# Performance work log

Measured on AMD Instinct MI355X. Metric: run time of the kernel, lower is better.

## Reference

```python
import jax, jax.numpy as jnp
import numpy as np

NUM_GRAPHS = 5 * 0 + 64  # number of graphs in the batch
NUM_CLASSES = 5


def gcn_conv(x, src, dst, W, b, n_nodes):
    """PyG GCNConv: x' = D^{-1/2} (A+I) D^{-1/2} x W + b (self-loops already in src/dst)."""
    h = x @ W  # [N, out]
    deg = jax.ops.segment_sum(jnp.ones(dst.shape, h.dtype), dst, num_segments=n_nodes)
    dinv = deg ** -0.5  # deg >= 1 thanks to self-loops
    norm = dinv[src] * dinv[dst]  # [E+N]
    msg = h[src] * norm[:, None]  # gather + normalize
    out = jax.ops.segment_sum(msg, dst, num_segments=n_nodes)  # scatter-add
    return out + b


def setup_inputs() -> dict:
    key = jax.random.key(0)
    ks = jax.random.split(key, 12)
    N, E, D_IN, D_H, D_F = 50000, 500000, 128, 256, 256
    x = jax.random.normal(ks[0], (N, D_IN), dtype=jnp.float32)
    edge_index = jax.random.randint(ks[1], (2, E), 0, N, dtype=jnp.int64)
    batch = jnp.sort(jax.random.randint(ks[2], (N,), 0, NUM_GRAPHS, dtype=jnp.int64))
    def lin(k, fi, fo):
        s = 1.0 / np.sqrt(fi)
        return jax.random.uniform(k, (fi, fo), jnp.float32, -s, s)
    return {
        "x": x, "edge_index": edge_index, "batch": batch,
        "W0": lin(ks[3], D_IN, D_H), "b0": jnp.zeros((D_H,), jnp.float32),
        "W1": lin(ks[4], D_H, D_H),  "b1": jnp.zeros((D_H,), jnp.float32),
        "W2": lin(ks[5], D_H, D_H),  "b2": jnp.zeros((D_H,), jnp.float32),
        "Wc1": lin(ks[6], D_H, D_F), "bc1": jnp.zeros((D_F,), jnp.float32),
        "Wc2": lin(ks[7], D_F, NUM_CLASSES), "bc2": jnp.zeros((NUM_CLASSES,), jnp.float32),
    }


def reference(x, edge_index, batch, W0, b0, W1, b1, W2, b2, Wc1, bc1, Wc2, bc2):
    n_nodes = x.shape[0]
    loops = jnp.arange(n_nodes, dtype=edge_index.dtype)
    src = jnp.concatenate([edge_index[0], loops])
    dst = jnp.concatenate([edge_index[1], loops])

    h = jax.nn.relu(gcn_conv(x, src, dst, W0, b0, n_nodes))
    h = jax.nn.relu(gcn_conv(h, src, dst, W1, b1, n_nodes))
    h = jax.nn.relu(gcn_conv(h, src, dst, W2, b2, n_nodes))

    # global_mean_pool over batch ids
    sums = jax.ops.segment_sum(h, batch, num_segments=NUM_GRAPHS)
    cnts = jax.ops.segment_sum(jnp.ones((n_nodes,), h.dtype), batch, num_segments=NUM_GRAPHS)
    g = sums / jnp.maximum(cnts, 1.0)[:, None]  # [NUM_GRAPHS, D_H]

    # classifier MLP (dropout inactive at eval)
    out = jax.nn.relu(g @ Wc1 + bc1) @ Wc2 + bc2
    return out
```

## Files before the change

### kernel.cpp

```cpp
#include <hip/hip_runtime.h>
#include <hip/hip_fp16.h>

typedef short s16x8 __attribute__((ext_vector_type(8)));
typedef float fx4 __attribute__((ext_vector_type(4)));

#define AS_G(p) ((const __attribute__((address_space(1))) void*)(p))
#define AS_L(p) ((__attribute__((address_space(3))) void*)(p))

struct __align__(8) half4 { __half2 lo, hi; };

__device__ inline unsigned short f32_to_bf16(float f) {
    unsigned int u = __float_as_uint(f);
    return (unsigned short)((u + 0x7fffu + ((u >> 16) & 1u)) >> 16);
}
__device__ inline float bf16_to_f32(unsigned short b) {
    return __uint_as_float(((unsigned int)b) << 16);
}
__device__ inline void split2(float a, unsigned short& hi, unsigned short& lo) {
    hi = f32_to_bf16(a);
    lo = f32_to_bf16(a - bf16_to_f32(hi));
}


__global__ void k_degx(const int* __restrict__ dst, int E, int* __restrict__ deg, int degB,
                       const float* __restrict__ x, __half* __restrict__ xh, int nx) {
    if (blockIdx.x < (unsigned)degB) {
        int i = blockIdx.x * 256 + threadIdx.x;
        if (i < E) atomicAdd(&deg[dst[i]], 1);
    } else {
        int i = (blockIdx.x - degB) * 1024 + threadIdx.x * 4;
        if (i < nx) {
            float4 v = *(const float4*)&x[i];
            __half2 h0(__float2half(v.x), __float2half(v.y));
            __half2 h1(__float2half(v.z), __float2half(v.w));
            *(__half2*)&xh[i] = h0;
            *(__half2*)&xh[i + 2] = h1;
        }
    }
}

__global__ void k_scan1w(const int* __restrict__ deg, int N, int nb,
                         int* __restrict__ part, int* __restrict__ bsum, float* __restrict__ dinv,
                         const float* __restrict__ W0, unsigned short* __restrict__ h0, unsigned short* __restrict__ l0,
                         const float* __restrict__ W1, unsigned short* __restrict__ h1, unsigned short* __restrict__ l1,
                         const float* __restrict__ W2, unsigned short* __restrict__ h2, unsigned short* __restrict__ l2,
                         int DIN, int DH) {
    __shared__ int s[256];
    if (blockIdx.x < (unsigned)nb) {
        int i = blockIdx.x * 256 + threadIdx.x;
        int v = (i < N) ? deg[i] : 0;
        if (i < N) dinv[i] = 1.0f / sqrtf((float)(v + 1));
        s[threadIdx.x] = v;
        __syncthreads();
        for (int off = 1; off < 256; off <<= 1) {
            int t = (threadIdx.x >= off) ? s[threadIdx.x - off] : 0;
            __syncthreads();
            s[threadIdx.x] += t;
            __syncthreads();
        }
        if (i < N) part[i] = s[threadIdx.x] - v;
        if (threadIdx.x == 255) bsum[blockIdx.x] = s[255];
    } else {
        int i = (blockIdx.x - nb) * 256 + threadIdx.x;
        const int n0 = DIN * DH, n1 = DH * DH;
        const float* W; unsigned short *hT, *lT; int K, li;
        if (i < n0) { W = W0; hT = h0; lT = l0; K = DIN; li = i; }
        else if (i < n0 + n1) { W = W1; hT = h1; lT = l1; K = DH; li = i - n0; }
        else if (i < n0 + 2 * n1) { W = W2; hT = h2; lT = l2; K = DH; li = i - n0 - n1; }
        else return;
        int k = li / DH, n = li - k * DH;
        unsigned short h, l;
        split2(W[li], h, l);
        hT[(size_t)n * K + k] = h;
        lT[(size_t)n * K + k] = l;
    }
}

__global__ void k_scan3(const int* __restrict__ part, const int* __restrict__ bsum, int nb,
                        int N, int E, int* __restrict__ rowptr, int* __restrict__ cursor) {
    __shared__ int s[256];
    const int t = threadIdx.x;
    s[t] = (t < nb && t < (int)blockIdx.x) ? bsum[t] : 0;
    __syncthreads();
    for (int off = 128; off > 0; off >>= 1) {
        if (t < off) s[t] += s[t + off];
        __syncthreads();
    }
    const int base = s[0];
    int i = blockIdx.x * 256 + t;
    if (i < N) {
        int v = part[i] + base;
        rowptr[i] = v;
        cursor[i] = v;
    }
    if (i == 0) rowptr[N] = E;
}

__global__ void k_fill(const int* __restrict__ src, const int* __restrict__ dst, int E,
                       const float* __restrict__ dinv, int* __restrict__ cursor,
                       int* __restrict__ col, float* __restrict__ nrm) {
    int e = blockIdx.x * blockDim.x + threadIdx.x;
    if (e < E) {
        int s = src[e], d = dst[e];
        int p = atomicAdd(&cursor[d], 1);
        col[p] = s;
        nrm[p] = dinv[s] * dinv[d];
    }
}


__global__ __launch_bounds__(256) void k_gemm_mfma(
    const unsigned short* __restrict__ Ahi, const unsigned short* __restrict__ Alo,
    const unsigned short* __restrict__ BhiT, const unsigned short* __restrict__ BloT,
    const float* __restrict__ bias, __half* __restrict__ C, int Nrows, int K) {
    __shared__ __align__(16) unsigned short smem[2][4][128 * 32];

    const int tid = threadIdx.x;
    const int wid = tid >> 6, lane = tid & 63;
    const int row0 = blockIdx.y * 128;
    const int col0 = blockIdx.x * 128;
    const int wrow = wid & 1, wcol = wid >> 1;
    const int quad = lane >> 4, l16 = lane & 15;

    const unsigned short* garr = (wid == 0) ? Ahi : (wid == 1) ? Alo : (wid == 2) ? BhiT : BloT;
    const bool isA = (wid < 2);

    const unsigned short* gp[8];
#pragma unroll
    for (int i = 0; i < 8; ++i) {
        int r = 16 * i + (lane >> 2);
        int s = lane & 3;
        int q = (s - (r >> 1)) & 3;
        int grow = isA ? min(row0 + r, Nrows - 1) : (col0 + r);
        gp[i] = garr + (size_t)grow * K + q * 8;
    }

    int aidx[4], bidx[4];
#pragma unroll
    for (int t = 0; t < 4; ++t) {
        int ra = wrow * 64 + t * 16 + l16;
        aidx[t] = ra * 32 + ((quad + (ra >> 1)) & 3) * 8;
        int rb = wcol * 64 + t * 16 + l16;
        bidx[t] = rb * 32 + ((quad + (rb >> 1)) & 3) * 8;
    }

    fx4 acc[4][4] = {};
    const int nch = K / 32;

#pragma unroll
    for (int i = 0; i < 8; ++i)
        __builtin_amdgcn_global_load_lds(AS_G(gp[i]), AS_L((char*)smem[0][wid] + i * 1024), 16, 0, 0);
    __syncthreads();

    for (int t = 0; t < nch; ++t) {
        const int buf = t & 1;
        if (t + 1 < nch) {
#pragma unroll
            for (int i = 0; i < 8; ++i)
                __builtin_amdgcn_global_load_lds(AS_G(gp[i] + (t + 1) * 32),
                                                 AS_L((char*)smem[1 - buf][wid] + i * 1024), 16, 0, 0);
        }

        const unsigned short* sAhi = smem[buf][0];
        const unsigned short* sAlo = smem[buf][1];
        const unsigned short* sBhi = smem[buf][2];
        const unsigned short* sBlo = smem[buf][3];

        s16x8 ah[4], al[4];
#pragma unroll
        for (int mi = 0; mi < 4; ++mi) {
            ah[mi] = *(const s16x8*)&sAhi[aidx[mi]];
            al[mi] = *(const s16x8*)&sAlo[aidx[mi]];
        }
#pragma unroll
        for (int nj = 0; nj < 4; ++nj) {
            s16x8 bh = *(const s16x8*)&sBhi[bidx[nj]];
            s16x8 bl = *(const s16x8*)&sBlo[bidx[nj]];
#pragma unroll
            for (int mi = 0; mi < 4; ++mi) {
                acc[mi][nj] = __builtin_amdgcn_mfma_f32_16x16x32_bf16(ah[mi], bh, acc[mi][nj], 0, 0, 0);
                acc[mi][nj] = __builtin_amdgcn_mfma_f32_16x16x32_bf16(ah[mi], bl, acc[mi][nj], 0, 0, 0);
                acc[mi][nj] = __builtin_amdgcn_mfma_f32_16x16x32_bf16(al[mi], bh, acc[mi][nj], 0, 0, 0);
            }
        }
        if (t + 1 < nch) __syncthreads();
    }

#pragma unroll
    for (int mi = 0; mi < 4; ++mi) {
        const int rbase = row0 + wrow * 64 + mi * 16 + quad * 4;
#pragma unroll
        for (int nj = 0; nj < 4; ++nj) {
            const int c = col0 + wcol * 64 + nj * 16 + l16;
            const float bc = bias[c];
#pragma unroll
            for (int reg = 0; reg < 4; ++reg) {
                int r = rbase + reg;
                if (r < Nrows) C[(size_t)r * 256 + c] = __float2half(fmaxf(acc[mi][nj][reg] + bc, 0.f));
            }
        }
    }
}

__global__ __launch_bounds__(256) void k_gemm_pool(
    const unsigned short* __restrict__ Ahi, const unsigned short* __restrict__ Alo,
    const unsigned short* __restrict__ BhiT, const unsigned short* __restrict__ BloT,
    const float* __restrict__ bias, const int* __restrict__ batch,
    float* __restrict__ gsum, int Nrows, int K) {
    __shared__ __align__(16) unsigned short smem[2][4][128 * 32];

    const int tid = threadIdx.x;
    const int wid = tid >> 6, lane = tid & 63;
    const int row0 = blockIdx.y * 128;
    const int col0 = blockIdx.x * 128;
    const int wrow = wid & 1, wcol = wid >> 1;
    const int quad = lane >> 4, l16 = lane & 15;

    const unsigned short* garr = (wid == 0) ? Ahi : (wid == 1) ? Alo : (wid == 2) ? BhiT : BloT;
    const bool isA = (wid < 2);

    const unsigned short* gp[8];
#pragma unroll
    for (int i = 0; i < 8; ++i) {
        int r = 16 * i + (lane >> 2);
        int s = lane & 3;
        int q = (s - (r >> 1)) & 3;
        int grow = isA ? min(row0 + r, Nrows - 1) : (col0 + r);
        gp[i] = garr + (size_t)grow * K + q * 8;
    }

    int aidx[4], bidx[4];
#pragma unroll
    for (int t = 0; t < 4; ++t) {
        int ra = wrow * 64 + t * 16 + l16;
        aidx[t] = ra * 32 + ((quad + (ra >> 1)) & 3) * 8;
        int rb = wcol * 64 + t * 16 + l16;
        bidx[t] = rb * 32 + ((quad + (rb >> 1)) & 3) * 8;
    }

    fx4 acc[4][4] = {};
    const int nch = K / 32;

#pragma unroll
    for (int i = 0; i < 8; ++i)
        __builtin_amdgcn_global_load_lds(AS_G(gp[i]), AS_L((char*)smem[0][wid] + i * 1024), 16, 0, 0);
    __syncthreads();

    for (int t = 0; t < nch; ++t) {
        const int buf = t & 1;
        if (t + 1 < nch) {
#pragma unroll
            for (int i = 0; i < 8; ++i)
                __builtin_amdgcn_global_load_lds(AS_G(gp[i] + (t + 1) * 32),
                                                 AS_L((char*)smem[1 - buf][wid] + i * 1024), 16, 0, 0);
        }

        const unsigned short* sAhi = smem[buf][0];
        const unsigned short* sAlo = smem[buf][1];
        const unsigned short* sBhi = smem[buf][2];
        const unsigned short* sBlo = smem[buf][3];

        s16x8 ah[4], al[4];
#pragma unroll
        for (int mi = 0; mi < 4; ++mi) {
            ah[mi] = *(const s16x8*)&sAhi[aidx[mi]];
            al[mi] = *(const s16x8*)&sAlo[aidx[mi]];
        }
#pragma unroll
        for (int nj = 0; nj < 4; ++nj) {
            s16x8 bh = *(const s16x8*)&sBhi[bidx[nj]];
            s16x8 bl = *(const s16x8*)&sBlo[bidx[nj]];
#pragma unroll
            for (int mi = 0; mi < 4; ++mi) {
                acc[mi][nj] = __builtin_amdgcn_mfma_f32_16x16x32_bf16(ah[mi], bh, acc[mi][nj], 0, 0, 0);
                acc[mi][nj] = __builtin_amdgcn_mfma_f32_16x16x32_bf16(ah[mi], bl, acc[mi][nj], 0, 0, 0);
                acc[mi][nj] = __builtin_amdgcn_mfma_f32_16x16x32_bf16(al[mi], bh, acc[mi][nj], 0, 0, 0);
            }
        }
        if (t + 1 < nch) __syncthreads();
    }

    int bg[4][4];
#pragma unroll
    for (int mi = 0; mi < 4; ++mi)
#pragma unroll
        for (int reg = 0; reg < 4; ++reg) {
            int r = row0 + wrow * 64 + mi * 16 + quad * 4 + reg;
            bg[mi][reg] = (r < Nrows) ? batch[r] : -1;
        }
    const int gfirst = batch[row0 < Nrows ? row0 : (Nrows - 1)];
    const int glast  = batch[min(row0 + 127, Nrows - 1)];

#pragma unroll
    for (int nj = 0; nj < 4; ++nj) {
        const int c = col0 + wcol * 64 + nj * 16 + l16;
        const float bc = bias[c];
        for (int g = gfirst; g <= glast; ++g) {
            float s = 0.f;
#pragma unroll
            for (int mi = 0; mi < 4; ++mi)
#pragma unroll
                for (int reg = 0; reg < 4; ++reg)
                    if (bg[mi][reg] == g) s += fmaxf(acc[mi][nj][reg] + bc, 0.f);
            s += __shfl_xor(s, 16);
            s += __shfl_xor(s, 32);
            if (quad == 0) atomicAdd(&gsum[g * 256 + c], s);
        }
    }
}


__global__ __launch_bounds__(256) void k_agg256(const __half* __restrict__ H, const int* __restrict__ rowptr,
                                                const int* __restrict__ col, const float* __restrict__ nrm,
                                                const float* __restrict__ dinv,
                                                unsigned short* __restrict__ outHi,
                                                unsigned short* __restrict__ outLo, int N) {
    const int wave = threadIdx.x >> 6, lane = threadIdx.x & 63;
    const int v = blockIdx.x * 4 + wave;
    if (v >= N) return;

    const float di = dinv[v];
    const float selfn = di * di;
    half4 hv = ((const half4*)&H[(size_t)v * 256])[lane];
    float2 s0 = __half22float2(hv.lo), s1 = __half22float2(hv.hi);
    float ax = selfn * s0.x, ay = selfn * s0.y, az = selfn * s1.x, aw = selfn * s1.y;

    int e = rowptr[v];
    const int end = rowptr[v + 1];
    for (; e + 8 <= end; e += 8) {
        int u[8]; float w[8]; half4 g[8];
#pragma unroll
        for (int j = 0; j < 8; ++j) { u[j] = col[e + j]; w[j] = nrm[e + j]; }
#pragma unroll
        for (int j = 0; j < 8; ++j) g[j] = ((const half4*)&H[(size_t)u[j] * 256])[lane];
#pragma unroll
        for (int j = 0; j < 8; ++j) {
            float2 f0 = __half22float2(g[j].lo), f1 = __half22float2(g[j].hi);
            ax += w[j] * f0.x; ay += w[j] * f0.y; az += w[j] * f1.x; aw += w[j] * f1.y;
        }
    }
    for (; e < end; ++e) {
        const int u = col[e];
        const float w = nrm[e];
        half4 g = ((const half4*)&H[(size_t)u * 256])[lane];
        float2 f0 = __half22float2(g.lo), f1 = __half22float2(g.hi);
        ax += w * f0.x; ay += w * f0.y; az += w * f1.x; aw += w * f1.y;
    }

    ushort4 hi4, lo4;
    split2(ax, hi4.x, lo4.x);
    split2(ay, hi4.y, lo4.y);
    split2(az, hi4.z, lo4.z);
    split2(aw, hi4.w, lo4.w);
    ((ushort4*)outHi)[(size_t)v * 64 + lane] = hi4;
    ((ushort4*)outLo)[(size_t)v * 64 + lane] = lo4;
}

__global__ __launch_bounds__(256) void k_agg128(const __half* __restrict__ X, const int* __restrict__ rowptr,
                                                const int* __restrict__ col, const float* __restrict__ nrm,
                                                const float* __restrict__ dinv,
                                                unsigned short* __restrict__ outHi,
                                                unsigned short* __restrict__ outLo, int N) {
    const int half = threadIdx.x >> 5, sub = threadIdx.x & 31;
    const int v = blockIdx.x * 8 + half;
    if (v >= N) return;

    const float di = dinv[v];
    const float selfn = di * di;
    half4 hv = ((const half4*)&X[(size_t)v * 128])[sub];
    float2 s0 = __half22float2(hv.lo), s1 = __half22float2(hv.hi);
    float ax = selfn * s0.x, ay = selfn * s0.y, az = selfn * s1.x, aw = selfn * s1.y;

    int e = rowptr[v];
    const int end = rowptr[v + 1];
    for (; e + 4 <= end; e += 4) {
        int u[4]; float w[4]; half4 g[4];
#pragma unroll
        for (int j = 0; j < 4; ++j) { u[j] = col[e + j]; w[j] = nrm[e + j]; }
#pragma unroll
        for (int j = 0; j < 4; ++j) g[j] = ((const half4*)&X[(size_t)u[j] * 128])[sub];
#pragma unroll
        for (int j = 0; j < 4; ++j) {
            float2 f0 = __half22float2(g[j].lo), f1 = __half22float2(g[j].hi);
            ax += w[j] * f0.x; ay += w[j] * f0.y; az += w[j] * f1.x; aw += w[j] * f1.y;
        }
    }
    for (; e < end; ++e) {
        const int u = col[e];
        const float w = nrm[e];
        half4 g = ((const half4*)&X[(size_t)u * 128])[sub];
        float2 f0 = __half22float2(g.lo), f1 = __half22float2(g.hi);
        ax += w * f0.x; ay += w * f0.y; az += w * f1.x; aw += w * f1.y;
    }

    ushort4 hi4, lo4;
    split2(ax, hi4.x, lo4.x);
    split2(ay, hi4.y, lo4.y);
    split2(az, hi4.z, lo4.z);
    split2(aw, hi4.w, lo4.w);
    ((ushort4*)outHi)[(size_t)v * 32 + sub] = hi4;
    ((ushort4*)outLo)[(size_t)v * 32 + sub] = lo4;
}


__global__ __launch_bounds__(256) void k_poolcls(const float* __restrict__ gsum, const int* __restrict__ batch,
                                                 int N,
                                                 const float* __restrict__ Wc1, const float* __restrict__ bc1,
                                                 const float* __restrict__ Wc2, const float* __restrict__ bc2,
                                                 float* __restrict__ out) {
    __shared__ float sg[256], sh[256];
    __shared__ int bounds[2];
    const int b = blockIdx.x, t = threadIdx.x;
    if (t < 2) {
        int target = b + t;
        int lo = 0, hi = N;
        while (lo < hi) {
            int mid = (lo + hi) >> 1;
            if (batch[mid] < target) lo = mid + 1; else hi = mid;
        }
        bounds[t] = lo;
    }
    __syncthreads();
    const float c = (float)(bounds[1] - bounds[0]);
    sg[t] = gsum[b * 256 + t] / fmaxf(c, 1.0f);
    __syncthreads();
    float acc = bc1[t];
    for (int k = 0; k < 256; ++k) acc += sg[k] * Wc1[k * 256 + t];
    sh[t] = fmaxf(acc, 0.f);
    __syncthreads();
    if (t < 5) {
        float o = bc2[t];
        for (int k = 0; k < 256; ++k) o += sh[k] * Wc2[k * 5 + t];
        out[b * 5 + t] = o;
    }
}


extern "C" void kernel_launch(void* const* d_in, const int* in_sizes, int n_in,
                              void* d_out, int out_size, void* d_ws, size_t ws_size,
                              hipStream_t stream) {
    const float* x    = (const float*)d_in[0];
    const int*   eidx = (const int*)d_in[1];
    const int*   batch= (const int*)d_in[2];
    const float* W0 = (const float*)d_in[3];  const float* b0 = (const float*)d_in[4];
    const float* W1 = (const float*)d_in[5];  const float* b1 = (const float*)d_in[6];
    const float* W2 = (const float*)d_in[7];  const float* b2 = (const float*)d_in[8];
    const float* Wc1= (const float*)d_in[9];  const float* bc1= (const float*)d_in[10];
    const float* Wc2= (const float*)d_in[11]; const float* bc2= (const float*)d_in[12];
    float* out = (float*)d_out;

    const int N   = in_sizes[2];
    const int E   = in_sizes[1] / 2;
    const int DIN = in_sizes[0] / N;
    const int DH  = in_sizes[4];
    const int* src = eidx;
    const int* dst = eidx + E;

    char* p = (char*)d_ws;
    auto alloc = [&](size_t bytes) {
        char* r = p;
        p += (bytes + 255) & ~(size_t)255;
        return (void*)r;
    };
    __half*         hbuf = (__half*)alloc((size_t)N * DH * 2);
    __half*         xh   = (__half*)alloc((size_t)N * DIN * 2);
    unsigned short* hhi  = (unsigned short*)alloc((size_t)N * DH * 2);
    unsigned short* hlo  = (unsigned short*)alloc((size_t)N * DH * 2);
    unsigned short* w0hi = (unsigned short*)alloc((size_t)DH * DIN * 2);
    unsigned short* w0lo = (unsigned short*)alloc((size_t)DH * DIN * 2);
    unsigned short* w1hi = (unsigned short*)alloc((size_t)DH * DH * 2);
    unsigned short* w1lo = (unsigned short*)alloc((size_t)DH * DH * 2);
    unsigned short* w2hi = (unsigned short*)alloc((size_t)DH * DH * 2);
    unsigned short* w2lo = (unsigned short*)alloc((size_t)DH * DH * 2);
    int*   deg   = (int*)alloc((size_t)N * 4);
    float* gsum  = (float*)alloc(64 * (size_t)DH * 4);
    float* dinv  = (float*)alloc((size_t)N * 4);
    int*   part  = (int*)alloc((size_t)N * 4);
    int*   bsum  = (int*)alloc(256 * 4);
    int*   rowptr= (int*)alloc((size_t)(N + 1) * 4);
    int*   cursor= (int*)alloc((size_t)N * 4);
    int*   col   = (int*)alloc((size_t)E * 4);
    float* nrm   = (float*)alloc((size_t)E * 4);

    hipMemsetAsync(deg, 0, (size_t)((char*)gsum - (char*)deg) + 64 * (size_t)DH * 4, stream);

    const int nb = (N + 255) / 256;
    const int wtot = DIN * DH + 2 * DH * DH;
    const int wb = (wtot + 255) / 256;
    const int degB = (E + 255) / 256;
    const int nx = N * DIN;
    const int xb = (nx + 1023) / 1024;

    k_degx  <<<degB + xb, 256, 0, stream>>>(dst, E, deg, degB, x, xh, nx);
    k_scan1w<<<nb + wb, 256, 0, stream>>>(deg, N, nb, part, bsum, dinv,
                                          W0, w0hi, w0lo, W1, w1hi, w1lo, W2, w2hi, w2lo, DIN, DH);
    k_scan3 <<<nb, 256, 0, stream>>>(part, bsum, nb, N, E, rowptr, cursor);
    k_fill  <<<(E + 255) / 256, 256, 0, stream>>>(src, dst, E, dinv, cursor, col, nrm);

    dim3 gemmGrid(DH / 128, (N + 127) / 128);

    k_agg128<<<(N + 7) / 8, 256, 0, stream>>>(xh, rowptr, col, nrm, dinv, hhi, hlo, N);
    k_gemm_mfma<<<gemmGrid, 256, 0, stream>>>(hhi, hlo, w0hi, w0lo, b0, hbuf, N, DIN);
    k_agg256<<<(N + 3) / 4, 256, 0, stream>>>(hbuf, rowptr, col, nrm, dinv, hhi, hlo, N);
    k_gemm_mfma<<<gemmGrid, 256, 0, stream>>>(hhi, hlo, w1hi, w1lo, b1, hbuf, N, DH);
    k_agg256<<<(N + 3) / 4, 256, 0, stream>>>(hbuf, rowptr, col, nrm, dinv, hhi, hlo, N);
    k_gemm_pool<<<gemmGrid, 256, 0, stream>>>(hhi, hlo, w2hi, w2lo, b2, batch, gsum, N, DH);

    k_poolcls<<<64, 256, 0, stream>>>(gsum, batch, N, Wc1, bc1, Wc2, bc2, out);
}
```

Measured before the change: 398.6 us.

## Switch GEMMs to fp16 with single-precision activations and split weights

Replaces the bf16 three-term split (Ahi*Bhi + Ahi*Blo + Alo*Bhi) with fp16 MFMA. Activations are kept as a single fp16 array and only the weights are split into hi/lo, so each step issues two MFMAs instead of three. The aggregation kernels now write one fp16 activation array instead of hi and lo arrays, which halves that write traffic and the GEMM's A-operand reads. The shared GEMM core drops the double-buffered LDS prefetch for a single buffer with load, sync, compute, sync, so global-load latency is no longer overlapped with compute, and accuracy now relies on fp16 activation precision.

```diff
diff --git a/kernel.cpp b/kernel.cpp
--- a/kernel.cpp
+++ b/kernel.cpp
@@ -1,7 +1,7 @@
 #include <hip/hip_runtime.h>
 #include <hip/hip_fp16.h>
 
-typedef short s16x8 __attribute__((ext_vector_type(8)));
+typedef _Float16 f16x8 __attribute__((ext_vector_type(8)));
 typedef float fx4 __attribute__((ext_vector_type(4)));
 
 #define AS_G(p) ((const __attribute__((address_space(1))) void*)(p))
@@ -9,16 +9,9 @@
 
 struct __align__(8) half4 { __half2 lo, hi; };
 
-__device__ inline unsigned short f32_to_bf16(float f) {
-    unsigned int u = __float_as_uint(f);
-    return (unsigned short)((u + 0x7fffu + ((u >> 16) & 1u)) >> 16);
-}
-__device__ inline float bf16_to_f32(unsigned short b) {
-    return __uint_as_float(((unsigned int)b) << 16);
-}
-__device__ inline void split2(float a, unsigned short& hi, unsigned short& lo) {
-    hi = f32_to_bf16(a);
-    lo = f32_to_bf16(a - bf16_to_f32(hi));
+__device__ inline void split2h(float a, __half& hi, __half& lo) {
+    hi = __float2half(a);
+    lo = __float2half(a - __half2float(hi));
 }
 
 
@@ -41,9 +34,9 @@
 
 __global__ void k_scan1w(const int* __restrict__ deg, int N, int nb,
                          int* __restrict__ part, int* __restrict__ bsum, float* __restrict__ dinv,
-                         const float* __restrict__ W0, unsigned short* __restrict__ h0, unsigned short* __restrict__ l0,
-                         const float* __restrict__ W1, unsigned short* __restrict__ h1, unsigned short* __restrict__ l1,
-                         const float* __restrict__ W2, unsigned short* __restrict__ h2, unsigned short* __restrict__ l2,
+                         const float* __restrict__ W0, __half* __restrict__ h0, __half* __restrict__ l0,
+                         const float* __restrict__ W1, __half* __restrict__ h1, __half* __restrict__ l1,
+                         const float* __restrict__ W2, __half* __restrict__ h2, __half* __restrict__ l2,
                          int DIN, int DH) {
     __shared__ int s[256];
     if (blockIdx.x < (unsigned)nb) {
@@ -63,14 +56,14 @@
     } else {
         int i = (blockIdx.x - nb) * 256 + threadIdx.x;
         const int n0 = DIN * DH, n1 = DH * DH;
-        const float* W; unsigned short *hT, *lT; int K, li;
+        const float* W; __half *hT, *lT; int K, li;
         if (i < n0) { W = W0; hT = h0; lT = l0; K = DIN; li = i; }
         else if (i < n0 + n1) { W = W1; hT = h1; lT = l1; K = DH; li = i - n0; }
         else if (i < n0 + 2 * n1) { W = W2; hT = h2; lT = l2; K = DH; li = i - n0 - n1; }
         else return;
         int k = li / DH, n = li - k * DH;
-        unsigned short h, l;
-        split2(W[li], h, l);
+        __half h, l;
+        split2h(W[li], h, l);
         hT[(size_t)n * K + k] = h;
         lT[(size_t)n * K + k] = l;
     }
@@ -109,31 +102,28 @@
 }
 
 
-__global__ __launch_bounds__(256) void k_gemm_mfma(
-    const unsigned short* __restrict__ Ahi, const unsigned short* __restrict__ Alo,
-    const unsigned short* __restrict__ BhiT, const unsigned short* __restrict__ BloT,
-    const float* __restrict__ bias, __half* __restrict__ C, int Nrows, int K) {
-    __shared__ __align__(16) unsigned short smem[2][4][128 * 32];
-
-    const int tid = threadIdx.x;
-    const int wid = tid >> 6, lane = tid & 63;
-    const int row0 = blockIdx.y * 128;
-    const int col0 = blockIdx.x * 128;
-    const int wrow = wid & 1, wcol = wid >> 1;
-    const int quad = lane >> 4, l16 = lane & 15;
-
-    const unsigned short* garr = (wid == 0) ? Ahi : (wid == 1) ? Alo : (wid == 2) ? BhiT : BloT;
-    const bool isA = (wid < 2);
-
-    const unsigned short* gp[8];
-#pragma unroll
-    for (int i = 0; i < 8; ++i) {
-        int r = 16 * i + (lane >> 2);
+__device__ __forceinline__ void gemm_core(
+    const __half* __restrict__ Aop, const __half* __restrict__ BhiT, const __half* __restrict__ BloT,
+    __half* smem, int Nrows, int K, int row0, int col0,
+    int wid, int lane, int wrow, int wcol, int quad, int l16, fx4 (&acc)[4][4]) {
+    const __half* gp[6];
+    int ldsoff[6];
+#pragma unroll
+    for (int j = 0; j < 6; ++j) {
+        int L = wid * 6 + j;
+        int arr = L >> 3, slot = L & 7;
+        int r = 16 * slot + (lane >> 2);
         int s = lane & 3;
         int q = (s - (r >> 1)) & 3;
-        int grow = isA ? min(row0 + r, Nrows - 1) : (col0 + r);
-        gp[i] = garr + (size_t)grow * K + q * 8;
-    }
+        const __half* garr = (arr == 0) ? Aop : (arr == 1) ? BhiT : BloT;
+        int grow = (arr == 0) ? min(row0 + r, Nrows - 1) : (col0 + r);
+        gp[j] = garr + (size_t)grow * K + q * 8;
+        ldsoff[j] = arr * 8192 + slot * 1024;
+    }
+
+    const __half* sA   = smem;
+    const __half* sBhi = smem + 128 * 32;
+    const __half* sBlo = smem + 2 * 128 * 32;
 
     int aidx[4], bidx[4];
 #pragma unroll
@@ -144,47 +134,41 @@
         bidx[t] = rb * 32 + ((quad + (rb >> 1)) & 3) * 8;
     }
 
+    for (int k0 = 0; k0 < K; k0 += 32) {
+#pragma unroll
+        for (int j = 0; j < 6; ++j)
+            __builtin_amdgcn_global_load_lds(AS_G(gp[j] + k0), AS_L((char*)smem + ldsoff[j]), 16, 0, 0);
+        __syncthreads();
+
+        f16x8 a[4];
+#pragma unroll
+        for (int mi = 0; mi < 4; ++mi) a[mi] = *(const f16x8*)&sA[aidx[mi]];
+#pragma unroll
+        for (int nj = 0; nj < 4; ++nj) {
+            f16x8 bh = *(const f16x8*)&sBhi[bidx[nj]];
+            f16x8 bl = *(const f16x8*)&sBlo[bidx[nj]];
+#pragma unroll
+            for (int mi = 0; mi < 4; ++mi) {
+                acc[mi][nj] = __builtin_amdgcn_mfma_f32_16x16x32_f16(a[mi], bh, acc[mi][nj], 0, 0, 0);
+                acc[mi][nj] = __builtin_amdgcn_mfma_f32_16x16x32_f16(a[mi], bl, acc[mi][nj], 0, 0, 0);
+            }
+        }
+        __syncthreads();
+    }
+}
+
+__global__ __launch_bounds__(256) void k_gemm_mfma(
+    const __half* __restrict__ Aop, const __half* __restrict__ BhiT, const __half* __restrict__ BloT,
+    const float* __restrict__ bias, __half* __restrict__ C, int Nrows, int K) {
+    __shared__ __align__(16) __half smem[3 * 128 * 32];
+    const int tid = threadIdx.x;
+    const int wid = tid >> 6, lane = tid & 63;
+    const int row0 = blockIdx.y * 128, col0 = blockIdx.x * 128;
+    const int wrow = wid & 1, wcol = wid >> 1;
+    const int quad = lane >> 4, l16 = lane & 15;
+
     fx4 acc[4][4] = {};
-    const int nch = K / 32;
-
-#pragma unroll
-    for (int i = 0; i < 8; ++i)
-        __builtin_amdgcn_global_load_lds(AS_G(gp[i]), AS_L((char*)smem[0][wid] + i * 1024), 16, 0, 0);
-    __syncthreads();
-
-    for (int t = 0; t < nch; ++t) {
-        const int buf = t & 1;
-        if (t + 1 < nch) {
-#pragma unroll
-            for (int i = 0; i < 8; ++i)
-                __builtin_amdgcn_global_load_lds(AS_G(gp[i] + (t + 1) * 32),
-                                                 AS_L((char*)smem[1 - buf][wid] + i * 1024), 16, 0, 0);
-        }
-
-        const unsigned short* sAhi = smem[buf][0];
-        const unsigned short* sAlo = smem[buf][1];
-        const unsigned short* sBhi = smem[buf][2];
-        const unsigned short* sBlo = smem[buf][3];
-
-        s16x8 ah[4], al[4];
-#pragma unroll
-        for (int mi = 0; mi < 4; ++mi) {
-            ah[mi] = *(const s16x8*)&sAhi[aidx[mi]];
-            al[mi] = *(const s16x8*)&sAlo[aidx[mi]];
-        }
-#pragma unroll
-        for (int nj = 0; nj < 4; ++nj) {
-            s16x8 bh = *(const s16x8*)&sBhi[bidx[nj]];
-            s16x8 bl = *(const s16x8*)&sBlo[bidx[nj]];
-#pragma unroll
-            for (int mi = 0; mi < 4; ++mi) {
-                acc[mi][nj] = __builtin_amdgcn_mfma_f32_16x16x32_bf16(ah[mi], bh, acc[mi][nj], 0, 0, 0);
-                acc[mi][nj] = __builtin_amdgcn_mfma_f32_16x16x32_bf16(ah[mi], bl, acc[mi][nj], 0, 0, 0);
-                acc[mi][nj] = __builtin_amdgcn_mfma_f32_16x16x32_bf16(al[mi], bh, acc[mi][nj], 0, 0, 0);
-            }
-        }
-        if (t + 1 < nch) __syncthreads();
-    }
+    gemm_core(Aop, BhiT, BloT, smem, Nrows, K, row0, col0, wid, lane, wrow, wcol, quad, l16, acc);
 
 #pragma unroll
     for (int mi = 0; mi < 4; ++mi) {
@@ -203,82 +187,18 @@
 }
 
 __global__ __launch_bounds__(256) void k_gemm_pool(
-    const unsigned short* __restrict__ Ahi, const unsigned short* __restrict__ Alo,
-    const unsigned short* __restrict__ BhiT, const unsigned short* __restrict__ BloT,
+    const __half* __restrict__ Aop, const __half* __restrict__ BhiT, const __half* __restrict__ BloT,
     const float* __restrict__ bias, const int* __restrict__ batch,
     float* __restrict__ gsum, int Nrows, int K) {
-    __shared__ __align__(16) unsigned short smem[2][4][128 * 32];
-
+    __shared__ __align__(16) __half smem[3 * 128 * 32];
     const int tid = threadIdx.x;
     const int wid = tid >> 6, lane = tid & 63;
-    const int row0 = blockIdx.y * 128;
-    const int col0 = blockIdx.x * 128;
+    const int row0 = blockIdx.y * 128, col0 = blockIdx.x * 128;
     const int wrow = wid & 1, wcol = wid >> 1;
     const int quad = lane >> 4, l16 = lane & 15;
 
-    const unsigned short* garr = (wid == 0) ? Ahi : (wid == 1) ? Alo : (wid == 2) ? BhiT : BloT;
-    const bool isA = (wid < 2);
-
-    const unsigned short* gp[8];
-#pragma unroll
-    for (int i = 0; i < 8; ++i) {
-        int r = 16 * i + (lane >> 2);
-        int s = lane & 3;
-        int q = (s - (r >> 1)) & 3;
-        int grow = isA ? min(row0 + r, Nrows - 1) : (col0 + r);
-        gp[i] = garr + (size_t)grow * K + q * 8;
-    }
-
-    int aidx[4], bidx[4];
-#pragma unroll
-    for (int t = 0; t < 4; ++t) {
-        int ra = wrow * 64 + t * 16 + l16;
-        aidx[t] = ra * 32 + ((quad + (ra >> 1)) & 3) * 8;
-        int rb = wcol * 64 + t * 16 + l16;
-        bidx[t] = rb * 32 + ((quad + (rb >> 1)) & 3) * 8;
-    }
-
     fx4 acc[4][4] = {};
-    const int nch = K / 32;
-
-#pragma unroll
-    for (int i = 0; i < 8; ++i)
-        __builtin_amdgcn_global_load_lds(AS_G(gp[i]), AS_L((char*)smem[0][wid] + i * 1024), 16, 0, 0);
-    __syncthreads();
-
-    for (int t = 0; t < nch; ++t) {
-        const int buf = t & 1;
-        if (t + 1 < nch) {
-#pragma unroll
-            for (int i = 0; i < 8; ++i)
-                __builtin_amdgcn_global_load_lds(AS_G(gp[i] + (t + 1) * 32),
-                                                 AS_L((char*)smem[1 - buf][wid] + i * 1024), 16, 0, 0);
-        }
-
-        const unsigned short* sAhi = smem[buf][0];
-        const unsigned short* sAlo = smem[buf][1];
-        const unsigned short* sBhi = smem[buf][2];
-        const unsigned short* sBlo = smem[buf][3];
-
-        s16x8 ah[4], al[4];
-#pragma unroll
-        for (int mi = 0; mi < 4; ++mi) {
-            ah[mi] = *(const s16x8*)&sAhi[aidx[mi]];
-            al[mi] = *(const s16x8*)&sAlo[aidx[mi]];
-        }
-#pragma unroll
-        for (int nj = 0; nj < 4; ++nj) {
-            s16x8 bh = *(const s16x8*)&sBhi[bidx[nj]];
-            s16x8 bl = *(const s16x8*)&sBlo[bidx[nj]];
-#pragma unroll
-            for (int mi = 0; mi < 4; ++mi) {
-                acc[mi][nj] = __builtin_amdgcn_mfma_f32_16x16x32_bf16(ah[mi], bh, acc[mi][nj], 0, 0, 0);
-                acc[mi][nj] = __builtin_amdgcn_mfma_f32_16x16x32_bf16(ah[mi], bl, acc[mi][nj], 0, 0, 0);
-                acc[mi][nj] = __builtin_amdgcn_mfma_f32_16x16x32_bf16(al[mi], bh, acc[mi][nj], 0, 0, 0);
-            }
-        }
-        if (t + 1 < nch) __syncthreads();
-    }
+    gemm_core(Aop, BhiT, BloT, smem, Nrows, K, row0, col0, wid, lane, wrow, wcol, quad, l16, acc);
 
     int bg[4][4];
 #pragma unroll
@@ -313,8 +233,7 @@
 __global__ __launch_bounds__(256) void k_agg256(const __half* __restrict__ H, const int* __restrict__ rowptr,
                                                 const int* __restrict__ col, const float* __restrict__ nrm,
                                                 const float* __restrict__ dinv,
-                                                unsigned short* __restrict__ outHi,
-                                                unsigned short* __restrict__ outLo, int N) {
+                                                __half* __restrict__ outA, int N) {
     const int wave = threadIdx.x >> 6, lane = threadIdx.x & 63;
     const int v = blockIdx.x * 4 + wave;
     if (v >= N) return;
@@ -347,20 +266,16 @@
         ax += w * f0.x; ay += w * f0.y; az += w * f1.x; aw += w * f1.y;
     }
 
-    ushort4 hi4, lo4;
-    split2(ax, hi4.x, lo4.x);
-    split2(ay, hi4.y, lo4.y);
-    split2(az, hi4.z, lo4.z);
-    split2(aw, hi4.w, lo4.w);
-    ((ushort4*)outHi)[(size_t)v * 64 + lane] = hi4;
-    ((ushort4*)outLo)[(size_t)v * 64 + lane] = lo4;
+    half4 o;
+    o.lo = __floats2half2_rn(ax, ay);
+    o.hi = __floats2half2_rn(az, aw);
+    ((half4*)outA)[(size_t)v * 64 + lane] = o;
 }
 
 __global__ __launch_bounds__(256) void k_agg128(const __half* __restrict__ X, const int* __restrict__ rowptr,
                                                 const int* __restrict__ col, const float* __restrict__ nrm,
                                                 const float* __restrict__ dinv,
-                                                unsigned short* __restrict__ outHi,
-                                                unsigned short* __restrict__ outLo, int N) {
+                                                __half* __restrict__ outA, int N) {
     const int half = threadIdx.x >> 5, sub = threadIdx.x & 31;
     const int v = blockIdx.x * 8 + half;
     if (v >= N) return;
@@ -393,13 +308,10 @@
         ax += w * f0.x; ay += w * f0.y; az += w * f1.x; aw += w * f1.y;
     }
 
-    ushort4 hi4, lo4;
-    split2(ax, hi4.x, lo4.x);
-    split2(ay, hi4.y, lo4.y);
-    split2(az, hi4.z, lo4.z);
-    split2(aw, hi4.w, lo4.w);
-    ((ushort4*)outHi)[(size_t)v * 32 + sub] = hi4;
-    ((ushort4*)outLo)[(size_t)v * 32 + sub] = lo4;
+    half4 o;
+    o.lo = __floats2half2_rn(ax, ay);
+    o.hi = __floats2half2_rn(az, aw);
+    ((half4*)outA)[(size_t)v * 32 + sub] = o;
 }
 
 
@@ -462,16 +374,15 @@
         p += (bytes + 255) & ~(size_t)255;
         return (void*)r;
     };
-    __half*         hbuf = (__half*)alloc((size_t)N * DH * 2);
-    __half*         xh   = (__half*)alloc((size_t)N * DIN * 2);
-    unsigned short* hhi  = (unsigned short*)alloc((size_t)N * DH * 2);
-    unsigned short* hlo  = (unsigned short*)alloc((size_t)N * DH * 2);
-    unsigned short* w0hi = (unsigned short*)alloc((size_t)DH * DIN * 2);
-    unsigned short* w0lo = (unsigned short*)alloc((size_t)DH * DIN * 2);
-    unsigned short* w1hi = (unsigned short*)alloc((size_t)DH * DH * 2);
-    unsigned short* w1lo = (unsigned short*)alloc((size_t)DH * DH * 2);
-    unsigned short* w2hi = (unsigned short*)alloc((size_t)DH * DH * 2);
-    unsigned short* w2lo = (unsigned short*)alloc((size_t)DH * DH * 2);
+    __half* hbuf = (__half*)alloc((size_t)N * DH * 2);
+    __half* ha   = (__half*)alloc((size_t)N * DH * 2);
+    __half* xh   = (__half*)alloc((size_t)N * DIN * 2);
+    __half* w0hi = (__half*)alloc((size_t)DH * DIN * 2);
+    __half* w0lo = (__half*)alloc((size_t)DH * DIN * 2);
+    __half* w1hi = (__half*)alloc((size_t)DH * DH * 2);
+    __half* w1lo = (__half*)alloc((size_t)DH * DH * 2);
+    __half* w2hi = (__half*)alloc((size_t)DH * DH * 2);
+    __half* w2lo = (__half*)alloc((size_t)DH * DH * 2);
     int*   deg   = (int*)alloc((size_t)N * 4);
     float* gsum  = (float*)alloc(64 * (size_t)DH * 4);
     float* dinv  = (float*)alloc((size_t)N * 4);
@@ -499,12 +410,12 @@
 
     dim3 gemmGrid(DH / 128, (N + 127) / 128);
 
-    k_agg128<<<(N + 7) / 8, 256, 0, stream>>>(xh, rowptr, col, nrm, dinv, hhi, hlo, N);
-    k_gemm_mfma<<<gemmGrid, 256, 0, stream>>>(hhi, hlo, w0hi, w0lo, b0, hbuf, N, DIN);
-    k_agg256<<<(N + 3) / 4, 256, 0, stream>>>(hbuf, rowptr, col, nrm, dinv, hhi, hlo, N);
-    k_gemm_mfma<<<gemmGrid, 256, 0, stream>>>(hhi, hlo, w1hi, w1lo, b1, hbuf, N, DH);
-    k_agg256<<<(N + 3) / 4, 256, 0, stream>>>(hbuf, rowptr, col, nrm, dinv, hhi, hlo, N);
-    k_gemm_pool<<<gemmGrid, 256, 0, stream>>>(hhi, hlo, w2hi, w2lo, b2, batch, gsum, N, DH);
+    k_agg128<<<(N + 7) / 8, 256, 0, stream>>>(xh, rowptr, col, nrm, dinv, ha, N);
+    k_gemm_mfma<<<gemmGrid, 256, 0, stream>>>(ha, w0hi, w0lo, b0, hbuf, N, DIN);
+    k_agg256<<<(N + 3) / 4, 256, 0, stream>>>(hbuf, rowptr, col, nrm, dinv, ha, N);
+    k_gemm_mfma<<<gemmGrid, 256, 0, stream>>>(ha, w1hi, w1lo, b1, hbuf, N, DH);
+    k_agg256<<<(N + 3) / 4, 256, 0, stream>>>(hbuf, rowptr, col, nrm, dinv, ha, N);
+    k_gemm_pool<<<gemmGrid, 256, 0, stream>>>(ha, w2hi, w2lo, b2, batch, gsum, N, DH);
 
     k_poolcls<<<64, 256, 0, stream>>>(gsum, batch, N, Wc1, bc1, Wc2, bc2, out);
 }
```

After: 369.6 us. 7.3% less time.
